# Optimization experiments

Hardware: AMD Instinct MI355X
Metric: run time of the kernel (lower is better)

The kernel has to match this reference:

```python
import jax, jax.numpy as jnp
import numpy as np

B, T, I, H, D, C, OUT = 32, 128, 64, 256, 32, 64, 32
DECAY = 0.99

def _lin(k, fi, fo):
    lim = 1.0 / np.sqrt(fi)
    kw, kb = jax.random.split(k)
    W = jax.random.uniform(kw, (fi, fo), minval=-lim, maxval=lim, dtype=jnp.float32)
    b = jax.random.uniform(kb, (fo,), minval=-lim, maxval=lim, dtype=jnp.float32)
    return W, b

def setup_inputs():
    key = jax.random.key(0)
    ks = jax.random.split(key, 12)
    x = jax.random.normal(ks[0], (B, T, I), dtype=jnp.float32)
    lengths = jax.random.randint(ks[1], (B,), 1, T + 1)
    W_dg1, b_dg1 = _lin(ks[2], I + H, D)
    W_dg2, b_dg2 = _lin(ks[3], D, D)
    W_e1, b_e1 = _lin(ks[4], 2 * I, H)
    W_e2, b_e2 = _lin(ks[5], H, H)
    W_ih, b_ih = _lin(ks[6], H, 3 * H)
    W_hh, b_hh = _lin(ks[7], H, 3 * H)
    W_f1, b_f1 = _lin(ks[8], H, H)
    W_f2, b_f2 = _lin(ks[9], H, C)
    return dict(x=x, lengths=lengths, out_lengths=OUT,
                W_dg1=W_dg1, b_dg1=b_dg1, W_dg2=W_dg2, b_dg2=b_dg2,
                W_e1=W_e1, b_e1=b_e1, W_e2=W_e2, b_e2=b_e2,
                W_ih=W_ih, b_ih=b_ih, W_hh=W_hh, b_hh=b_hh,
                W_f1=W_f1, b_f1=b_f1, W_f2=W_f2, b_f2=b_f2)

def _forward(x, lengths, out_lengths, W_dg1, b_dg1, W_dg2, b_dg2, W_e1, b_e1, W_e2, b_e2,
             W_ih, b_ih, W_hh, b_hh, W_f1, b_f1, W_f2, b_f2):
    Bs, Ts, Is = x.shape
    Ds = W_dg2.shape[1]
    Hs = W_e2.shape[1]
    decay = DECAY ** jnp.arange(1, Ds + 1, dtype=x.dtype)  # [D]
    d_idx = jnp.arange(Ds)
    gkey = jax.random.key(42)
    g_enc = jax.random.gumbel(jax.random.fold_in(gkey, 0), (Ts, Bs, Ds), x.dtype)
    g_dec = jax.random.gumbel(jax.random.fold_in(gkey, 1), (out_lengths, Bs, Ds), x.dtype)
    masks = (jnp.arange(Ts)[None, :] < lengths[:, None]).astype(x.dtype)  # [B,T]

    def gumbel_softmax_hard(logits, g):
        # F.gumbel_softmax(..., tau=1.0, hard=True) straight-through estimator
        y_soft = jax.nn.softmax(logits + g, axis=-1)
        y_hard = jax.nn.one_hot(jnp.argmax(y_soft, axis=-1), Ds, dtype=logits.dtype)
        return y_hard + y_soft - jax.lax.stop_gradient(y_soft)

    def gru_cell(xin, h):
        # torch.nn.GRUCell gate order: r, z, n
        gi = xin @ W_ih + b_ih
        gh = h @ W_hh + b_hh
        i_r, i_z, i_n = jnp.split(gi, 3, axis=-1)
        h_r, h_z, h_n = jnp.split(gh, 3, axis=-1)
        r = jax.nn.sigmoid(i_r + h_r)
        z = jax.nn.sigmoid(i_z + h_z)
        n = jnp.tanh(i_n + r * h_n)
        return (1.0 - z) * n + z * h

    def step_core(buf, h, x_t, g_t, mem_t):
        cell_in = jnp.concatenate([x_t, h], axis=-1)
        logits = jax.nn.elu(cell_in @ W_dg1 + b_dg1) @ W_dg2 + b_dg2
        gate = gumbel_softmax_hard(logits, g_t)  # [B,D]
        # shift buffer along dim 1 (new[:, :-1] = old[:, 1:], last slot zeroed)
        new_buf = jnp.concatenate([buf[:, 1:], jnp.zeros_like(buf[:, :1])], axis=1)
        upd = x_t[:, None, :] * decay[None, :, None] * gate[:, :, None]  # [B,D,I]
        new_buf = new_buf.at[:, d_idx, d_idx].set(upd)  # diagonal scatter-assign
        rnn_in = jnp.concatenate([x_t, mem_t], axis=-1)
        rnn_in = jax.nn.elu(rnn_in @ W_e1 + b_e1) @ W_e2 + b_e2
        return new_buf, gru_cell(rnn_in, h)

    buf0 = jnp.zeros((Bs, Ds + 1, Ds, Is), x.dtype)
    h0 = jnp.zeros((Bs, Hs), x.dtype)

    def enc_step(carry, inp):
        buf, h = carry
        x_t, m_t, g_t = inp
        mem_t = buf[:, 0].sum(axis=1)  # [B,I]
        buf, nh = step_core(buf, h, x_t, g_t, mem_t)
        h = m_t[:, None] * nh + (1.0 - m_t[:, None]) * h
        return (buf, h), None

    (buf, h), _ = jax.lax.scan(enc_step, (buf0, h0),
                               (jnp.swapaxes(x, 0, 1), masks.T, g_enc))

    x_zero = jnp.zeros((Bs, Is), x.dtype)

    def dec_step(carry, g_t):
        buf, h = carry
        # get_current_memory(slide=True): roll -1 along dim1 with last slot zeroed
        buf = jnp.concatenate([buf[:, 1:], jnp.zeros_like(buf[:, :1])], axis=1)
        mem_t = buf[:, 0].sum(axis=1)
        buf, nh = step_core(buf, h, x_zero, g_t, mem_t)
        out = jax.nn.relu(nh @ W_f1 + b_f1) @ W_f2 + b_f2
        return (buf, nh), out

    _, outs = jax.lax.scan(dec_step, (buf, h), g_dec)  # [OUT,B,C]
    return jnp.swapaxes(outs, 0, 1)  # [B,OUT,C]

def reference(x, lengths, out_lengths, W_dg1, b_dg1, W_dg2, b_dg2, W_e1, b_e1, W_e2, b_e2,
              W_ih, b_ih, W_hh, b_hh, W_f1, b_f1, W_f2, b_f2):
    return _forward(x, lengths, out_lengths, W_dg1, b_dg1, W_dg2, b_dg2, W_e1, b_e1,
                    W_e2, b_e2, W_ih, b_ih, W_hh, b_hh, W_f1, b_f1, W_f2, b_f2)
```

## Files before the change

### kernel.cpp

```cpp
#include <hip/hip_runtime.h>
#include <math.h>


#define kB 32
#define kT 128
#define kI 64
#define kH 256
#define kD 32
#define kC 64
#define kOut 32
#define kSteps (kT + kOut)
#define NB 89
#define NTHR 256
#define NT_ALL (NB * NTHR)

#define WS_FL    384
#define WS_H     1856
#define WS_SEL   (WS_H + 4*8192)
#define WS_MEM   (WS_SEL + 128)
#define WS_NZ    (WS_MEM + kB*kSteps*kI)
#define WS_LIN   WS_NZ
#define WS_O1    (WS_LIN + 4*8192)
#define WS_W2    (WS_O1 + 4*8192)
#define WS_B2    (WS_W2 + kH*3*kH)
#define WS_G     (WS_B2 + 3*kH)
#define WS_P     (WS_G + kT*kB*kD)
#define WS_ZERO_BYTES ((size_t)WS_NZ * sizeof(float))

__device__ __forceinline__ float cload(const float* p) {
  return __hip_atomic_load(p, __ATOMIC_RELAXED, __HIP_MEMORY_SCOPE_AGENT);
}
__device__ __forceinline__ void cstore(float* p, float v) {
  __hip_atomic_store(p, v, __ATOMIC_RELAXED, __HIP_MEMORY_SCOPE_AGENT);
}
__device__ __forceinline__ int cload_i(const int* p) {
  return __hip_atomic_load(p, __ATOMIC_RELAXED, __HIP_MEMORY_SCOPE_AGENT);
}
__device__ __forceinline__ void cstore_i(int* p, int v) {
  __hip_atomic_store(p, v, __ATOMIC_RELAXED, __HIP_MEMORY_SCOPE_AGENT);
}
__device__ __forceinline__ float4 cload4(const float* p) {
  float4 r;
  asm volatile("global_load_dwordx4 %0, %1, off sc0 sc1" : "=v"(r) : "v"(p));
  return r;
}
__device__ __forceinline__ void waitvm() {
  asm volatile("s_waitcnt vmcnt(0)" ::: "memory");
}

__device__ __forceinline__ void poll(const int* FL, int tid,
                                     int tH, int tDG, int tE, int tF1, int tF2) {
  int thr;
  if      (tid < 32) thr = tH;
  else if (tid == 32) thr = tDG;
  else if (tid < 65) thr = tE;
  else if (tid < 81) thr = tF1;
  else if (tid < 89) thr = tF2;
  else thr = 0;
  const int* p = FL + tid * 16;
  for (;;) {
    int ok = (thr <= 0) || (cload_i(p) >= thr);
    if (__syncthreads_count(ok) == NTHR) return;
    __builtin_amdgcn_s_sleep(2);
  }
}
__device__ __forceinline__ void setflag(int* FL, int tid, int idx, int val) {
  waitvm();
  __syncthreads();
  if (tid == 0) cstore_i(FL + idx * 16, val);
}

__device__ __forceinline__ void tf2x32(unsigned k0, unsigned k1,
                                       unsigned x0, unsigned x1,
                                       unsigned& o0, unsigned& o1) {
  unsigned ks2 = k0 ^ k1 ^ 0x1BD11BDAu;
  unsigned v0 = x0 + k0, v1 = x1 + k1;
#define TFR(r) { v0 += v1; v1 = (v1 << (r)) | (v1 >> (32-(r))); v1 ^= v0; }
  TFR(13) TFR(15) TFR(26) TFR(6)   v0 += k1;  v1 += ks2 + 1u;
  TFR(17) TFR(29) TFR(16) TFR(24)  v0 += ks2; v1 += k0  + 2u;
  TFR(13) TFR(15) TFR(26) TFR(6)   v0 += k0;  v1 += k1  + 3u;
  TFR(17) TFR(29) TFR(16) TFR(24)  v0 += k1;  v1 += ks2 + 4u;
  TFR(13) TFR(15) TFR(26) TFR(6)   v0 += ks2; v1 += k0  + 5u;
#undef TFR
  o0 = v0; o1 = v1;
}
__device__ __forceinline__ float bits_to_gumbel(unsigned bits) {
  float f = __uint_as_float((bits >> 9) | 0x3F800000u) - 1.0f;
  float u = f + 1.17549435e-38f;
  return -logf(-logf(u));
}

__device__ __forceinline__ void gridbar_full(unsigned* u, unsigned target) {
  __syncthreads();
  if (threadIdx.x == 0) {
    __threadfence();
    __hip_atomic_fetch_add(&u[320], 1u, __ATOMIC_ACQ_REL, __HIP_MEMORY_SCOPE_AGENT);
    while (__hip_atomic_load(&u[320], __ATOMIC_RELAXED, __HIP_MEMORY_SCOPE_AGENT) < target)
      __builtin_amdgcn_s_sleep(1);
    __threadfence();
  }
  __syncthreads();
}

__device__ __forceinline__ float elu1(float v) { return v > 0.f ? v : expm1f(v); }

__global__ __launch_bounds__(NTHR)
void delay_rnn(const float* __restrict__ x, const int* __restrict__ lengths,
               const float* __restrict__ W_dg1, const float* __restrict__ b_dg1,
               const float* __restrict__ W_dg2, const float* __restrict__ b_dg2,
               const float* __restrict__ W_e1,  const float* __restrict__ b_e1,
               const float* __restrict__ W_e2,  const float* __restrict__ b_e2,
               const float* __restrict__ W_ih,  const float* __restrict__ b_ih,
               const float* __restrict__ W_hh,  const float* __restrict__ b_hh,
               const float* __restrict__ W_f1,  const float* __restrict__ b_f1,
               const float* __restrict__ W_f2,  const float* __restrict__ b_f2,
               float* __restrict__ out, float* __restrict__ ws) {
  const int tid = threadIdx.x;
  const int bid = blockIdx.x;
  const int gid = bid * NTHR + tid;

  unsigned* baru = (unsigned*)ws;
  int*   FL    = (int*)(ws + WS_FL);
  float* hBuf  = ws + WS_H;
  int*   selG  = (int*)(ws + WS_SEL);
  float* mem   = ws + WS_MEM;
  float* linB  = ws + WS_LIN;
  float* o1B   = ws + WS_O1;
  float* W2g   = ws + WS_W2;
  float* B2g   = ws + WS_B2;
  float* g     = ws + WS_G;
  float* Pg    = ws + WS_P;

  __shared__ float S[35264];
  __shared__ float lgarr[1056];
  __shared__ float sb1[32], sb2[32], dec_sh[32];
  __shared__ int   sel[32], len_s[32];

  {
    unsigned k0, k1;
    tf2x32(0u, 42u, 0u, 0u, k0, k1);
    for (int i = gid; i < kT * kB * kD; i += NT_ALL) {
      unsigned a, b;
      tf2x32(k0, k1, 0u, (unsigned)i, a, b);
      g[i] = bits_to_gumbel(a ^ b);
    }
  }
  for (int idx = gid; idx < kH * 3 * kH; idx += NT_ALL) {
    int k = idx / (3 * kH), n = idx % (3 * kH);
    const float* wr = W_e2 + k * kH;
    float s0 = 0, s1 = 0, s2 = 0, s3 = 0;
    for (int m = 0; m < kH; m += 4) {
      float4 wv = *(const float4*)(wr + m);
      s0 += wv.x * W_ih[(m    ) * 3 * kH + n];
      s1 += wv.y * W_ih[(m + 1) * 3 * kH + n];
      s2 += wv.z * W_ih[(m + 2) * 3 * kH + n];
      s3 += wv.w * W_ih[(m + 3) * 3 * kH + n];
    }
    W2g[idx] = ((s0 + s1) + (s2 + s3));
  }
  for (int n = gid; n < 3 * kH; n += NT_ALL) {
    float s = b_ih[n];
    for (int m = 0; m < kH; ++m) s += b_e2[m] * W_ih[m * 3 * kH + n];
    B2g[n] = s;
  }
  for (int idx = gid; idx < kT * kB * kH; idx += NT_ALL) {
    int s = idx >> 13, r = idx & 8191, b = r >> 8, j = r & 255;
    const float* xr = x + (b * kT + s) * kI;
    float a0 = 0, a1 = 0, a2 = 0, a3 = 0;
    for (int k = 0; k < 64; k += 4) {
      float4 xv = *(const float4*)(xr + k);
      a0 += xv.x * W_e1[(64 + k) * 256 + j];
      a1 += xv.y * W_e1[(65 + k) * 256 + j];
      a2 += xv.z * W_e1[(66 + k) * 256 + j];
      a3 += xv.w * W_e1[(67 + k) * 256 + j];
    }
    Pg[idx] = ((a0 + a1) + (a2 + a3));
  }

  gridbar_full(baru, NB);

  if (bid < 32) {
    float* whh = S; float* w2 = S + 6240;
    const int jb = bid * 8;
    for (int i = tid; i < 6144; i += NTHR) {
      int gg = i >> 11, r = i & 2047, jj = r >> 8, k = r & 255;
      whh[(gg * 8 + jj) * 260 + k] = W_hh[k * 768 + gg * 256 + jb + jj];
      w2 [(gg * 8 + jj) * 260 + k] = W2g [k * 768 + gg * 256 + jb + jj];
    }
    if (tid < 24) { int gg = tid / 8, jj = tid % 8;
      sb1[tid] = b_hh[gg * 256 + jb + jj];
      sb2[tid] = B2g [gg * 256 + jb + jj];
    }
    if (tid < 32) len_s[tid] = lengths[tid];
    __syncthreads();

    float* sH = S + 12480; float* sLin = S + 20800;
    float* red = S + 29120;
    for (int s = 0; s < kSteps; ++s) {
      int tDG = (s >= 1) ? (s < kT ? s : kT) : 0;
      int tF1 = (s >= kT + 4) ? (s - 2) : 0;
      poll(FL, tid, s, tDG, s + 1, tF1, 0);

      const float* hR = hBuf + (s & 3) * 8192;
      const float* lR = linB + (s & 3) * 8192;
      const bool useC = (s >= 1 && s < kT);
      const float4* P4 = (const float4*)(Pg + (s - 1) * 8192);
      const int* selR = selG + ((s - 1) & 3) * 32;
      float4 th[8], tl[8], tp[8];
      int tsel[8];
      #pragma unroll
      for (int u8 = 0; u8 < 8; ++u8) {
        int i4 = (tid + u8 * 256) * 4;
        th[u8] = cload4(hR + i4);
        tl[u8] = cload4(lR + i4);
      }
      if (useC) {
        #pragma unroll
        for (int u8 = 0; u8 < 8; ++u8) {
          int idx = tid + u8 * 256; int b = idx >> 6, k4 = idx & 63;
          tp[u8] = P4[b * 64 + k4];
          tsel[u8] = cload_i(&selR[b]);
        }
      }
      waitvm();
      #pragma unroll
      for (int u8 = 0; u8 < 8; ++u8) {
        int idx = tid + u8 * 256; int b = idx >> 6, k4 = idx & 63;
        *(float4*)&sH[b * 260 + k4 * 4] = th[u8];
        float cx = 0.f, cy = 0.f, cz = 0.f, cw = 0.f;
        if (useC && tsel[u8] == 0) {
          cx = 0.99f * tp[u8].x; cy = 0.99f * tp[u8].y;
          cz = 0.99f * tp[u8].z; cw = 0.99f * tp[u8].w;
        }
        float4 v;
        v.x = elu1(tl[u8].x + cx);
        v.y = elu1(tl[u8].y + cy);
        v.z = elu1(tl[u8].z + cz);
        v.w = elu1(tl[u8].w + cw);
        *(float4*)&sLin[b * 260 + k4 * 4] = v;
      }
      __syncthreads();
      const float4* sH4 = (const float4*)sH;
      const float4* sL4 = (const float4*)sLin;
      const float4* wh4 = (const float4*)whh;
      const float4* w24 = (const float4*)w2;
      const int c  = tid & 7;
      const int b4 = (tid >> 3) & 7;
      const int kq = tid >> 6;
      float acc[24];
      #pragma unroll
      for (int a = 0; a < 24; ++a) acc[a] = 0.f;
      for (int kk = 0; kk < 16; ++kk) {
        int k4 = kq * 16 + kk;
        float4 wr[6];
        #pragma unroll
        for (int gg = 0; gg < 3; ++gg) {
          wr[gg]     = wh4[(gg * 8 + c) * 65 + k4];
          wr[3 + gg] = w24[(gg * 8 + c) * 65 + k4];
        }
        #pragma unroll
        for (int bi = 0; bi < 4; ++bi) {
          int b = bi * 8 + b4;
          float4 h4 = sH4[b * 65 + k4];
          float4 l4 = sL4[b * 65 + k4];
          #pragma unroll
          for (int gg = 0; gg < 3; ++gg) {
            float4 w = wr[gg];
            acc[bi * 6 + gg]     += h4.x * w.x + h4.y * w.y + h4.z * w.z + h4.w * w.w;
            w = wr[3 + gg];
            acc[bi * 6 + 3 + gg] += l4.x * w.x + l4.y * w.y + l4.z * w.z + l4.w * w.w;
          }
        }
      }
      #pragma unroll
      for (int bi = 0; bi < 4; ++bi)
        #pragma unroll
        for (int rr = 0; rr < 6; ++rr)
          red[kq * 1536 + rr * 256 + (bi * 8 + b4) * 8 + c] = acc[bi * 6 + rr];
      __syncthreads();
      {
        int b = tid >> 3, cc = tid & 7, jg = bid * 8 + cc;
        int lo = b * 8 + cc;
        float dots[6];
        #pragma unroll
        for (int rr = 0; rr < 6; ++rr)
          dots[rr] = (red[rr * 256 + lo] + red[1536 + rr * 256 + lo]) +
                     (red[3072 + rr * 256 + lo] + red[4608 + rr * 256 + lo]);
        float ghr = dots[0] + sb1[cc];
        float ghz = dots[1] + sb1[8 + cc];
        float ghn = dots[2] + sb1[16 + cc];
        float gir = dots[3] + sb2[cc];
        float giz = dots[4] + sb2[8 + cc];
        float gin = dots[5] + sb2[16 + cc];
        float r = 1.f / (1.f + expf(-(gir + ghr)));
        float z = 1.f / (1.f + expf(-(giz + ghz)));
        float n = tanhf(gin + r * ghn);
        float hold = sH[b * 260 + jg];
        float nh = (1.f - z) * n + z * hold;
        float hv = (s < kT) ? ((s < len_s[b]) ? nh : hold) : nh;
        cstore(&hBuf[((s + 1) & 3) * 8192 + b * 256 + jg], hv);
      }
      setflag(FL, tid, bid, s + 1);
    }
  }
  else if (bid < 64) {
    float* we1 = S;
    const int jb = (bid - 32) * 8;
    for (int i = tid; i < 1024; i += NTHR) {
      int jj = i >> 7, k = i & 127;
      we1[jj * 132 + k] = W_e1[k * 256 + jb + jj];
    }
    if (tid < 8) sb1[tid] = b_e1[jb + tid];
    __syncthreads();

    float* sx = S + 1056; float* sm = S + 3232;
    for (int e = 0; e < kSteps; ++e) {
      int tDG = e - 1 < 0 ? 0 : (e - 1 > kT ? kT : e - 1);
      poll(FL, tid, e - 2, tDG, 0, 0, 0);

      const bool encx = (e < kT);
      float4 tm[2];
      #pragma unroll
      for (int u2 = 0; u2 < 2; ++u2) {
        int idx = tid + u2 * 256; int b = idx >> 4, k4 = idx & 15;
        tm[u2] = cload4(mem + (b * kSteps + e) * kI + k4 * 4);
      }
      waitvm();
      #pragma unroll
      for (int u2 = 0; u2 < 2; ++u2) {
        int idx = tid + u2 * 256; int b = idx >> 4, k4 = idx & 15;
        *(float4*)&sm[b * 68 + k4 * 4] = tm[u2];
        if (encx)
          *(float4*)&sx[b * 68 + k4 * 4] =
              *(const float4*)(x + (b * kT + e) * kI + k4 * 4);
      }
      __syncthreads();
      const int b = tid >> 3, jj = tid & 7;
      const float4* sx4 = (const float4*)sx;
      const float4* sm4 = (const float4*)sm;
      const float4* w4p = (const float4*)we1;
      float a0 = 0, a1 = 0, a2 = 0, a3 = 0;
      if (encx) {
        for (int k4 = 0; k4 < 16; ++k4) {
          float4 xv = sx4[b * 17 + k4], w = w4p[jj * 33 + k4];
          a0 += xv.x * w.x; a1 += xv.y * w.y; a2 += xv.z * w.z; a3 += xv.w * w.w;
        }
      }
      for (int k4 = 0; k4 < 16; ++k4) {
        float4 mv = sm4[b * 17 + k4], w = w4p[jj * 33 + 16 + k4];
        a0 += mv.x * w.x; a1 += mv.y * w.y; a2 += mv.z * w.z; a3 += mv.w * w.w;
      }
      cstore(&linB[(e & 3) * 8192 + b * 256 + jb + jj],
             ((a0 + a1) + (a2 + a3)) + sb1[jj]);
      __syncthreads();
      setflag(FL, tid, 33 + (bid - 32), e + 1);
    }
  }
  else if (bid < 80) {
    float* wf1 = S;
    const int jb = (bid - 64) * 16;
    for (int i = tid; i < 4096; i += NTHR) {
      int jj = i >> 8, k = i & 255;
      wf1[jj * 260 + k] = W_f1[k * 256 + jb + jj];
    }
    if (tid < 16) sb1[tid] = b_f1[jb + tid];
    __syncthreads();

    float* sHf = S + 4160; float* red = S + 12480;
    for (int s = kT + 1; s <= kSteps; ++s) {
      int tF2 = (s >= kT + 5) ? (s - 2) : 0;
      poll(FL, tid, s, 0, 0, 0, tF2);

      const float* hR = hBuf + (s & 3) * 8192;
      float4 th[8];
      #pragma unroll
      for (int u8 = 0; u8 < 8; ++u8) th[u8] = cload4(hR + (tid + u8 * 256) * 4);
      waitvm();
      #pragma unroll
      for (int u8 = 0; u8 < 8; ++u8) {
        int idx = tid + u8 * 256; int b = idx >> 6, k4 = idx & 63;
        *(float4*)&sHf[b * 260 + k4 * 4] = th[u8];
      }
      __syncthreads();
      const float4* sH4 = (const float4*)sHf;
      const float4* w4p = (const float4*)wf1;
      const int cq = tid & 3, b4 = (tid >> 2) & 7, kq = tid >> 5;
      float acc[16];
      #pragma unroll
      for (int a = 0; a < 16; ++a) acc[a] = 0.f;
      for (int kk = 0; kk < 8; ++kk) {
        int k4 = kq * 8 + kk;
        float4 wr[4];
        #pragma unroll
        for (int ci = 0; ci < 4; ++ci) wr[ci] = w4p[(cq * 4 + ci) * 65 + k4];
        #pragma unroll
        for (int bi = 0; bi < 4; ++bi) {
          float4 h4 = sH4[(bi * 8 + b4) * 65 + k4];
          #pragma unroll
          for (int ci = 0; ci < 4; ++ci) {
            float4 w = wr[ci];
            acc[bi * 4 + ci] += h4.x * w.x + h4.y * w.y + h4.z * w.z + h4.w * w.w;
          }
        }
      }
      #pragma unroll
      for (int bi = 0; bi < 4; ++bi)
        #pragma unroll
        for (int ci = 0; ci < 4; ++ci)
          red[kq * 512 + (bi * 4 + ci) * 32 + cq * 8 + b4] = acc[bi * 4 + ci];
      __syncthreads();
      #pragma unroll
      for (int u2 = 0; u2 < 2; ++u2) {
        int o = tid * 2 + u2; int b = o >> 4, col = o & 15;
        int gg = ((b >> 3) * 4 + (col & 3)) * 32 + (col >> 2) * 8 + (b & 7);
        float v = 0.f;
        #pragma unroll
        for (int kq2 = 0; kq2 < 8; ++kq2) v += red[kq2 * 512 + gg];
        v += sb1[col];
        cstore(&o1B[(s & 3) * 8192 + b * 256 + (bid - 64) * 16 + col],
               v > 0.f ? v : 0.f);
      }
      __syncthreads();
      setflag(FL, tid, 65 + (bid - 64), s + 1);
    }
  }
  else if (bid < 88) {
    float* wf2 = S;
    const int cb = (bid - 80) * 8;
    for (int i = tid; i < 2048; i += NTHR) {
      int cc = i >> 8, k = i & 255;
      wf2[cc * 260 + k] = W_f2[k * 64 + cb + cc];
    }
    if (tid < 8) sb2[tid] = b_f2[cb + tid];
    __syncthreads();

    float* sO = S + 2080; float* red = S + 10400;
    for (int s = kT + 2; s <= kSteps + 1; ++s) {
      poll(FL, tid, 0, 0, 0, s, 0);

      const float* oR = o1B + ((s - 1) & 3) * 8192;
      float4 to[8];
      #pragma unroll
      for (int u8 = 0; u8 < 8; ++u8) to[u8] = cload4(oR + (tid + u8 * 256) * 4);
      waitvm();
      #pragma unroll
      for (int u8 = 0; u8 < 8; ++u8) {
        int idx = tid + u8 * 256; int b = idx >> 6, k4 = idx & 63;
        *(float4*)&sO[b * 260 + k4 * 4] = to[u8];
      }
      __syncthreads();
      const float4* sO4 = (const float4*)sO;
      const float4* w4p = (const float4*)wf2;
      const int c = tid & 7, b4 = (tid >> 3) & 7, kq = tid >> 6;
      float acc[4] = {0.f, 0.f, 0.f, 0.f};
      for (int kk = 0; kk < 16; ++kk) {
        int k4 = kq * 16 + kk;
        float4 w = w4p[c * 65 + k4];
        #pragma unroll
        for (int bi = 0; bi < 4; ++bi) {
          float4 o4 = sO4[(bi * 8 + b4) * 65 + k4];
          acc[bi] += o4.x * w.x + o4.y * w.y + o4.z * w.z + o4.w * w.w;
        }
      }
      #pragma unroll
      for (int bi = 0; bi < 4; ++bi)
        red[kq * 256 + bi * 64 + b4 * 8 + c] = acc[bi];
      __syncthreads();
      { int b = tid >> 3, col = tid & 7;
        int gg = (b >> 3) * 64 + (b & 7) * 8 + col;
        float v = (red[gg] + red[256 + gg]) + (red[512 + gg] + red[768 + gg]);
        out[(b * kOut + (s - 2 - kT)) * kC + (bid - 80) * 8 + col] =
            v + sb2[col];
      }
      __syncthreads();
      setflag(FL, tid, 81 + (bid - 80), s + 1);
    }
  }
  else {
    float* wdg1 = S; float* wdg2 = S + 10368;
    for (int i = tid; i < 10240; i += NTHR) {
      int j = i / 320, k = i % 320;
      wdg1[j * 324 + k] = W_dg1[k * 32 + j];
    }
    for (int i = tid; i < 1024; i += NTHR) wdg2[i] = W_dg2[i];
    if (tid < 32) { sb1[tid] = b_dg1[tid]; sb2[tid] = b_dg2[tid];
                    dec_sh[tid] = powf(0.99f, (float)(tid + 1)); }
    __syncthreads();

    float* sXH = S + 11392;
    float* red = S + 21760;
    float* l1s = S + 25856;
    for (int s = 0; s < kT; ++s) {
      poll(FL, tid, s, 0, 0, 0, 0);

      const float* hR = hBuf + (s & 3) * 8192;
      float4 th[8];
      #pragma unroll
      for (int u8 = 0; u8 < 8; ++u8) th[u8] = cload4(hR + (tid + u8 * 256) * 4);
      waitvm();
      #pragma unroll
      for (int u8 = 0; u8 < 8; ++u8) {
        int idx = tid + u8 * 256; int b = idx >> 6, k4 = idx & 63;
        *(float4*)&sXH[b * 324 + 64 + k4 * 4] = th[u8];
      }
      #pragma unroll
      for (int u2 = 0; u2 < 2; ++u2) {
        int idx = tid + u2 * 256; int b = idx >> 4, k4 = idx & 15;
        *(float4*)&sXH[b * 324 + k4 * 4] =
            *(const float4*)(x + (b * kT + s) * kI + k4 * 4);
      }
      __syncthreads();
      {
        const float4* sA4 = (const float4*)sXH;
        const float4* wd4 = (const float4*)wdg1;
        const int cq = tid & 7, b4 = (tid >> 3) & 7, kq = tid >> 6;
        float acc[16];
        #pragma unroll
        for (int a = 0; a < 16; ++a) acc[a] = 0.f;
        for (int kk = 0; kk < 20; ++kk) {
          int k4 = kq * 20 + kk;
          float4 wr[4];
          #pragma unroll
          for (int ci = 0; ci < 4; ++ci) wr[ci] = wd4[(cq * 4 + ci) * 81 + k4];
          #pragma unroll
          for (int bi = 0; bi < 4; ++bi) {
            float4 a4 = sA4[(bi * 8 + b4) * 81 + k4];
            #pragma unroll
            for (int ci = 0; ci < 4; ++ci) {
              float4 w = wr[ci];
              acc[bi * 4 + ci] += a4.x * w.x + a4.y * w.y + a4.z * w.z + a4.w * w.w;
            }
          }
        }
        #pragma unroll
        for (int bi = 0; bi < 4; ++bi)
          #pragma unroll
          for (int ci = 0; ci < 4; ++ci)
            red[kq * 1024 + (ci * 4 + bi) * 64 + cq * 8 + b4] = acc[bi * 4 + ci];
        __syncthreads();
        #pragma unroll
        for (int u4 = 0; u4 < 4; ++u4) {
          int o = tid * 4 + u4; int b = o >> 5, col = o & 31;
          int ci = col & 3, cq2 = col >> 2, bi = b >> 3, b42 = b & 7;
          int f = (ci * 4 + bi) * 64 + cq2 * 8 + b42;
          float v = (red[f] + red[1024 + f]) + (red[2048 + f] + red[3072 + f]);
          l1s[b * 36 + col] = elu1(v + sb1[col]);
        }
      }
      __syncthreads();
      for (int it = 0; it < 4; ++it) {
        int i = tid + it * 256; int b = i >> 5, j = i & 31;
        float sv = sb2[j];
        for (int k = 0; k < 32; ++k) sv += l1s[b * 36 + k] * wdg2[k * 32 + j];
        lgarr[b * 33 + j] = sv + g[(s * 32 + b) * 32 + j];
      }
      __syncthreads();
      if (tid < 32) {
        float best = lgarr[tid * 33]; int bi = 0;
        for (int j = 1; j < 32; ++j) {
          float v = lgarr[tid * 33 + j];
          if (v > best) { best = v; bi = j; }
        }
        sel[tid] = bi;
      }
      __syncthreads();
      if (tid < 32) cstore_i(&selG[(s & 3) * 32 + tid], sel[tid]);
      for (int it = 0; it < 8; ++it) {
        int i = tid + it * 256; int b = i >> 6, ii = i & 63;
        int d = sel[b];
        if (d > 0) {
          int c = s + 1 + d, e = -1;
          if (c < kT) e = c;
          else { int rr = c - kT - 1;
                 if (rr >= 0 && !(rr & 1)) { int kk = rr >> 1; if (kk < kOut) e = kT + kk; } }
          if (e >= 0) {
            float* p = &mem[(b * kSteps + e) * kI + ii];
            cstore(p, cload(p) + sXH[b * 324 + ii] * dec_sh[d]);
          }
        }
      }
      setflag(FL, tid, 32, s + 1);
    }
  }
}

extern "C" void kernel_launch(void* const* d_in, const int* in_sizes, int n_in,
                              void* d_out, int out_size, void* d_ws, size_t ws_size,
                              hipStream_t stream) {
  (void)in_sizes; (void)n_in; (void)out_size; (void)ws_size;
  const float* x      = (const float*)d_in[0];
  const int*   lens   = (const int*)  d_in[1];
  const float* W_dg1  = (const float*)d_in[3];
  const float* b_dg1  = (const float*)d_in[4];
  const float* W_dg2  = (const float*)d_in[5];
  const float* b_dg2  = (const float*)d_in[6];
  const float* W_e1   = (const float*)d_in[7];
  const float* b_e1   = (const float*)d_in[8];
  const float* W_e2   = (const float*)d_in[9];
  const float* b_e2   = (const float*)d_in[10];
  const float* W_ih   = (const float*)d_in[11];
  const float* b_ih   = (const float*)d_in[12];
  const float* W_hh   = (const float*)d_in[13];
  const float* b_hh   = (const float*)d_in[14];
  const float* W_f1   = (const float*)d_in[15];
  const float* b_f1   = (const float*)d_in[16];
  const float* W_f2   = (const float*)d_in[17];
  const float* b_f2   = (const float*)d_in[18];

  hipMemsetAsync(d_ws, 0, WS_ZERO_BYTES, stream);
  delay_rnn<<<dim3(NB), dim3(NTHR), 0, stream>>>(
      x, lens, W_dg1, b_dg1, W_dg2, b_dg2, W_e1, b_e1, W_e2, b_e2,
      W_ih, b_ih, W_hh, b_hh, W_f1, b_f1, W_f2, b_f2,
      (float*)d_out, (float*)d_ws);
}
```

Before: 1.936 ms.

## Precompute x-part of delay-gate layer; retile GRU GEMV with 8-way k split

```diff
diff --git a/kernel.cpp b/kernel.cpp
--- a/kernel.cpp
+++ b/kernel.cpp
@@ -25,6 +25,7 @@
 #define WS_B2    (WS_W2 + kH*3*kH)
 #define WS_G     (WS_B2 + 3*kH)
 #define WS_P     (WS_G + kT*kB*kD)
+#define WS_PDG   (WS_P + kT*kB*kH)
 #define WS_ZERO_BYTES ((size_t)WS_NZ * sizeof(float))
 
 __device__ __forceinline__ float cload(const float* p) {
@@ -61,7 +62,7 @@
   for (;;) {
     int ok = (thr <= 0) || (cload_i(p) >= thr);
     if (__syncthreads_count(ok) == NTHR) return;
-    __builtin_amdgcn_s_sleep(2);
+    __builtin_amdgcn_s_sleep(1);
   }
 }
 __device__ __forceinline__ void setflag(int* FL, int tid, int idx, int val) {
@@ -104,7 +105,7 @@
 
 __device__ __forceinline__ float elu1(float v) { return v > 0.f ? v : expm1f(v); }
 
-__global__ __launch_bounds__(NTHR)
+__global__ __launch_bounds__(NTHR, 1)
 void delay_rnn(const float* __restrict__ x, const int* __restrict__ lengths,
                const float* __restrict__ W_dg1, const float* __restrict__ b_dg1,
                const float* __restrict__ W_dg2, const float* __restrict__ b_dg2,
@@ -130,8 +131,9 @@
   float* B2g   = ws + WS_B2;
   float* g     = ws + WS_G;
   float* Pg    = ws + WS_P;
-
-  __shared__ float S[35264];
+  float* PDG   = ws + WS_PDG;
+
+  __shared__ float S[29120];
   __shared__ float lgarr[1056];
   __shared__ float sb1[32], sb2[32], dec_sh[32];
   __shared__ int   sel[32], len_s[32];
@@ -176,6 +178,19 @@
     }
     Pg[idx] = ((a0 + a1) + (a2 + a3));
   }
+  for (int idx = gid; idx < kT * kB * kD; idx += NT_ALL) {
+    int s = idx >> 10, r = idx & 1023, b = r >> 5, j = r & 31;
+    const float* xr = x + (b * kT + s) * kI;
+    float a0 = 0, a1 = 0, a2 = 0, a3 = 0;
+    for (int k = 0; k < 64; k += 4) {
+      float4 xv = *(const float4*)(xr + k);
+      a0 += xv.x * W_dg1[(k    ) * 32 + j];
+      a1 += xv.y * W_dg1[(k + 1) * 32 + j];
+      a2 += xv.z * W_dg1[(k + 2) * 32 + j];
+      a3 += xv.w * W_dg1[(k + 3) * 32 + j];
+    }
+    PDG[idx] = ((a0 + a1) + (a2 + a3));
+  }
 
   gridbar_full(baru, NB);
 
@@ -195,7 +210,7 @@
     __syncthreads();
 
     float* sH = S + 12480; float* sLin = S + 20800;
-    float* red = S + 29120;
+    float* red = S + 12480;
     for (int s = 0; s < kSteps; ++s) {
       int tDG = (s >= 1) ? (s < kT ? s : kT) : 0;
       int tF1 = (s >= kT + 4) ? (s - 2) : 0;
@@ -244,60 +259,78 @@
       const float4* sL4 = (const float4*)sLin;
       const float4* wh4 = (const float4*)whh;
       const float4* w24 = (const float4*)w2;
-      const int c  = tid & 7;
-      const int b4 = (tid >> 3) & 7;
-      const int kq = tid >> 6;
-      float acc[24];
-      #pragma unroll
-      for (int a = 0; a < 24; ++a) acc[a] = 0.f;
-      for (int kk = 0; kk < 16; ++kk) {
-        int k4 = kq * 16 + kk;
-        float4 wr[6];
-        #pragma unroll
-        for (int gg = 0; gg < 3; ++gg) {
-          wr[gg]     = wh4[(gg * 8 + c) * 65 + k4];
-          wr[3 + gg] = w24[(gg * 8 + c) * 65 + k4];
-        }
+      const int cgrp = tid & 3;
+      const int b4   = (tid >> 2) & 7;
+      const int kq   = tid >> 5;
+      float acc[48];
+      #pragma unroll
+      for (int a = 0; a < 48; ++a) acc[a] = 0.f;
+      for (int kk = 0; kk < 8; ++kk) {
+        int k4 = kq * 8 + kk;
+        float4 wh[6], ww[6];
+        #pragma unroll
+        for (int gg = 0; gg < 3; ++gg)
+          #pragma unroll
+          for (int ci = 0; ci < 2; ++ci) {
+            wh[gg * 2 + ci] = wh4[(gg * 8 + cgrp * 2 + ci) * 65 + k4];
+            ww[gg * 2 + ci] = w24[(gg * 8 + cgrp * 2 + ci) * 65 + k4];
+          }
         #pragma unroll
         for (int bi = 0; bi < 4; ++bi) {
           int b = bi * 8 + b4;
           float4 h4 = sH4[b * 65 + k4];
           float4 l4 = sL4[b * 65 + k4];
           #pragma unroll
+          for (int ci = 0; ci < 2; ++ci)
+            #pragma unroll
+            for (int gg = 0; gg < 3; ++gg) {
+              float4 w = wh[gg * 2 + ci];
+              acc[((bi * 2 + ci) * 3 + gg) * 2] +=
+                  h4.x * w.x + h4.y * w.y + h4.z * w.z + h4.w * w.w;
+              w = ww[gg * 2 + ci];
+              acc[((bi * 2 + ci) * 3 + gg) * 2 + 1] +=
+                  l4.x * w.x + l4.y * w.y + l4.z * w.z + l4.w * w.w;
+            }
+        }
+      }
+      float holdv;
+      { int b = tid >> 3, cc = tid & 7; holdv = sH[b * 260 + bid * 8 + cc]; }
+      __syncthreads();
+      #pragma unroll
+      for (int bi = 0; bi < 4; ++bi)
+        #pragma unroll
+        for (int ci = 0; ci < 2; ++ci)
+          #pragma unroll
           for (int gg = 0; gg < 3; ++gg) {
-            float4 w = wr[gg];
-            acc[bi * 6 + gg]     += h4.x * w.x + h4.y * w.y + h4.z * w.z + h4.w * w.w;
-            w = wr[3 + gg];
-            acc[bi * 6 + 3 + gg] += l4.x * w.x + l4.y * w.y + l4.z * w.z + l4.w * w.w;
+            int b = bi * 8 + b4, col = cgrp * 2 + ci;
+            red[kq * 1543 + (gg * 2) * 257 + b * 8 + col] =
+                acc[((bi * 2 + ci) * 3 + gg) * 2];
+            red[kq * 1543 + (gg * 2 + 1) * 257 + b * 8 + col] =
+                acc[((bi * 2 + ci) * 3 + gg) * 2 + 1];
           }
-        }
-      }
-      #pragma unroll
-      for (int bi = 0; bi < 4; ++bi)
-        #pragma unroll
-        for (int rr = 0; rr < 6; ++rr)
-          red[kq * 1536 + rr * 256 + (bi * 8 + b4) * 8 + c] = acc[bi * 6 + rr];
       __syncthreads();
       {
         int b = tid >> 3, cc = tid & 7, jg = bid * 8 + cc;
-        int lo = b * 8 + cc;
         float dots[6];
         #pragma unroll
-        for (int rr = 0; rr < 6; ++rr)
-          dots[rr] = (red[rr * 256 + lo] + red[1536 + rr * 256 + lo]) +
-                     (red[3072 + rr * 256 + lo] + red[4608 + rr * 256 + lo]);
+        for (int rr = 0; rr < 6; ++rr) {
+          float v = 0.f;
+          #pragma unroll
+          for (int kq2 = 0; kq2 < 8; ++kq2)
+            v += red[kq2 * 1543 + rr * 257 + tid];
+          dots[rr] = v;
+        }
         float ghr = dots[0] + sb1[cc];
-        float ghz = dots[1] + sb1[8 + cc];
-        float ghn = dots[2] + sb1[16 + cc];
-        float gir = dots[3] + sb2[cc];
-        float giz = dots[4] + sb2[8 + cc];
+        float gir = dots[1] + sb2[cc];
+        float ghz = dots[2] + sb1[8 + cc];
+        float giz = dots[3] + sb2[8 + cc];
+        float ghn = dots[4] + sb1[16 + cc];
         float gin = dots[5] + sb2[16 + cc];
         float r = 1.f / (1.f + expf(-(gir + ghr)));
         float z = 1.f / (1.f + expf(-(giz + ghz)));
         float n = tanhf(gin + r * ghn);
-        float hold = sH[b * 260 + jg];
-        float nh = (1.f - z) * n + z * hold;
-        float hv = (s < kT) ? ((s < len_s[b]) ? nh : hold) : nh;
+        float nh = (1.f - z) * n + z * holdv;
+        float hv = (s < kT) ? ((s < len_s[b]) ? nh : holdv) : nh;
         cstore(&hBuf[((s + 1) & 3) * 8192 + b * 256 + jg], hv);
       }
       setflag(FL, tid, bid, s + 1);
@@ -477,19 +510,21 @@
     }
   }
   else {
-    float* wdg1 = S; float* wdg2 = S + 10368;
-    for (int i = tid; i < 10240; i += NTHR) {
-      int j = i / 320, k = i % 320;
-      wdg1[j * 324 + k] = W_dg1[k * 32 + j];
+    float* wdg1h = S;
+    float* wdg2  = S + 8320;
+    for (int i = tid; i < 8192; i += NTHR) {
+      int j = i >> 8, k = i & 255;
+      wdg1h[j * 260 + k] = W_dg1[(64 + k) * 32 + j];
     }
     for (int i = tid; i < 1024; i += NTHR) wdg2[i] = W_dg2[i];
     if (tid < 32) { sb1[tid] = b_dg1[tid]; sb2[tid] = b_dg2[tid];
                     dec_sh[tid] = powf(0.99f, (float)(tid + 1)); }
     __syncthreads();
 
-    float* sXH = S + 11392;
-    float* red = S + 21760;
-    float* l1s = S + 25856;
+    float* sDH = S + 9344;
+    float* sx  = S + 17664;
+    float* red = S + 19840;
+    float* l1s = S + 23936;
     for (int s = 0; s < kT; ++s) {
       poll(FL, tid, s, 0, 0, 0, 0);
 
@@ -501,30 +536,30 @@
       #pragma unroll
       for (int u8 = 0; u8 < 8; ++u8) {
         int idx = tid + u8 * 256; int b = idx >> 6, k4 = idx & 63;
-        *(float4*)&sXH[b * 324 + 64 + k4 * 4] = th[u8];
+        *(float4*)&sDH[b * 260 + k4 * 4] = th[u8];
       }
       #pragma unroll
       for (int u2 = 0; u2 < 2; ++u2) {
         int idx = tid + u2 * 256; int b = idx >> 4, k4 = idx & 15;
-        *(float4*)&sXH[b * 324 + k4 * 4] =
+        *(float4*)&sx[b * 68 + k4 * 4] =
             *(const float4*)(x + (b * kT + s) * kI + k4 * 4);
       }
       __syncthreads();
       {
-        const float4* sA4 = (const float4*)sXH;
-        const float4* wd4 = (const float4*)wdg1;
+        const float4* sA4 = (const float4*)sDH;
+        const float4* wd4 = (const float4*)wdg1h;
         const int cq = tid & 7, b4 = (tid >> 3) & 7, kq = tid >> 6;
         float acc[16];
         #pragma unroll
         for (int a = 0; a < 16; ++a) acc[a] = 0.f;
-        for (int kk = 0; kk < 20; ++kk) {
-          int k4 = kq * 20 + kk;
+        for (int kk = 0; kk < 16; ++kk) {
+          int k4 = kq * 16 + kk;
           float4 wr[4];
           #pragma unroll
-          for (int ci = 0; ci < 4; ++ci) wr[ci] = wd4[(cq * 4 + ci) * 81 + k4];
+          for (int ci = 0; ci < 4; ++ci) wr[ci] = wd4[(ci * 8 + cq) * 65 + k4];
           #pragma unroll
           for (int bi = 0; bi < 4; ++bi) {
-            float4 a4 = sA4[(bi * 8 + b4) * 81 + k4];
+            float4 a4 = sA4[(bi * 8 + b4) * 65 + k4];
             #pragma unroll
             for (int ci = 0; ci < 4; ++ci) {
               float4 w = wr[ci];
@@ -541,10 +576,11 @@
         #pragma unroll
         for (int u4 = 0; u4 < 4; ++u4) {
           int o = tid * 4 + u4; int b = o >> 5, col = o & 31;
-          int ci = col & 3, cq2 = col >> 2, bi = b >> 3, b42 = b & 7;
+          int ci = col >> 3, cq2 = col & 7, bi = b >> 3, b42 = b & 7;
           int f = (ci * 4 + bi) * 64 + cq2 * 8 + b42;
           float v = (red[f] + red[1024 + f]) + (red[2048 + f] + red[3072 + f]);
-          l1s[b * 36 + col] = elu1(v + sb1[col]);
+          l1s[b * 36 + col] =
+              elu1(v + PDG[(s * 32 + b) * 32 + col] + sb1[col]);
         }
       }
       __syncthreads();
@@ -575,7 +611,7 @@
                  if (rr >= 0 && !(rr & 1)) { int kk = rr >> 1; if (kk < kOut) e = kT + kk; } }
           if (e >= 0) {
             float* p = &mem[(b * kSteps + e) * kI + ii];
-            cstore(p, cload(p) + sXH[b * 324 + ii] * dec_sh[d]);
+            cstore(p, cload(p) + sx[b * 68 + ii] * dec_sh[d]);
           }
         }
       }
```

After: 1.973 ms. Within noise of the previous version (+1.9%).
